# Performance work log

Hardware: AMD Instinct MI355X
Metric: run time of the kernel (lower is better)

Reference implementation:

```python
import jax, jax.numpy as jnp
import numpy as np

B, N, C, H = 128, 256, 512, 2
HD = C // H  # head_dim == num_patches == N by construction of the module's einsums
ALPHA = 3.0


def _safe_pow(x, p):
    # x >= 0 (post-relu); avoid 0**p corner issues while matching x**p exactly for x>0
    pos = x > 0
    return jnp.where(pos, jnp.where(pos, x, 1.0) ** p, 0.0)


def setup_inputs() -> dict:
    key = jax.random.key(0)
    ks = jax.random.split(key, 12)
    s = 0.02
    return {
        "x": jax.random.normal(ks[0], (B, N, C), jnp.float32),
        "Wq": jax.random.normal(ks[1], (C, C), jnp.float32) * s,
        "bq": jnp.zeros((C,), jnp.float32),
        "Wk": jax.random.normal(ks[2], (C, C), jnp.float32) * s,
        "bk": jnp.zeros((C,), jnp.float32),
        "Wvs": jax.random.normal(ks[3], (C, C // 2), jnp.float32) * s,
        "bvs": jnp.zeros((C // 2,), jnp.float32),
        "Wvc": jax.random.normal(ks[4], (C, C // 2), jnp.float32) * s,
        "bvc": jnp.zeros((C // 2,), jnp.float32),
        "power": jnp.ones((1, H, 1, HD), jnp.float32),
        "W_s": jax.random.uniform(ks[5], (N, HD // 2), jnp.float32),
        "W_c": jax.random.uniform(ks[6], (N, HD // 2), jnp.float32),
        "Wp": jax.random.normal(ks[7], (C, C), jnp.float32) * s,
        "bp": jnp.zeros((C,), jnp.float32),
    }


def reference(x, Wq, bq, Wk, bk, Wvs, bvs, Wvc, bvc, power, W_s, W_c, Wp, bp):
    b, n, c = x.shape
    h, hd = H, c // H
    # projections -> [B, H, N, hd] (or hd//2 for values)
    q = (x @ Wq + bq).reshape(b, n, h, hd).transpose(0, 2, 1, 3)
    k = (x @ Wk + bk).reshape(b, n, h, hd).transpose(0, 2, 1, 3)
    v_s = (x @ Wvs + bvs).reshape(b, n, h, hd // 2).transpose(0, 2, 1, 3)
    v_c = (x @ Wvc + bvc).reshape(b, n, h, hd // 2).transpose(0, 2, 1, 3)

    power_val = 1.0 + ALPHA * jax.nn.sigmoid(power)  # [1,H,1,hd]
    q_pos = _safe_pow(jax.nn.relu(q), power_val)
    q_neg = _safe_pow(jax.nn.relu(-q), power_val)
    k_pos = _safe_pow(jax.nn.relu(k), power_val)
    k_neg = _safe_pow(jax.nn.relu(-k), power_val)

    # kv_s = einsum(k_pos,v_s)+einsum(k_neg,v_s) == einsum(k_pos+k_neg, v_s); same for kv_c
    k_abs = k_pos + k_neg
    q_abs = q_pos + q_neg
    kv_s = jnp.einsum('bhnj,bhjd->bhnd', k_abs, v_s)
    q_s_context = jnp.einsum('bhni,bhid->bhnd', q_abs, kv_s)
    kv_c = jnp.einsum('bhnj,bhjd->bhnd', k_abs, v_c)
    q_c_context = jnp.einsum('bhni,bhid->bhnd', q_abs, kv_c)

    kp_sum = k_pos.sum(-1)  # [B,H,N]
    kn_sum = k_neg.sum(-1)
    denom_s = jnp.einsum('bhni,bhi->bhn', q_pos, kp_sum) + jnp.einsum('bhni,bhi->bhn', q_neg, kn_sum)
    denom_c = jnp.einsum('bhni,bhi->bhn', q_pos, kn_sum) + jnp.einsum('bhni,bhi->bhn', q_neg, kp_sum)

    attn_s = q_s_context / (denom_s[..., None] + 1e-6) * W_s  # W_s: [N, hd//2]
    attn_c = q_c_context / (denom_c[..., None] + 1e-6) * W_c

    out = jnp.concatenate([attn_s, attn_c], axis=-1)  # [B,H,N,hd]
    out = out.transpose(0, 2, 1, 3).reshape(b, n, c)
    return out @ Wp + bp
```

## Files before the change

### kernel.cpp

```cpp
#include <hip/hip_runtime.h>
#include <hip/hip_bf16.h>
#include <math.h>

typedef unsigned int u32;
typedef short bf16x8 __attribute__((ext_vector_type(8)));
typedef float f32x4 __attribute__((ext_vector_type(4)));
typedef u32 u32x4 __attribute__((ext_vector_type(4)));

__device__ __forceinline__ float bf2f(short s) {
    u32 u = ((u32)(unsigned short)s) << 16;
    return __builtin_bit_cast(float, u);
}
__device__ __forceinline__ short f2bf(float f) {
    u32 u = __builtin_bit_cast(u32, f);
    u32 r = u + 0x7fffu + ((u >> 16) & 1u);
    return (short)(r >> 16);
}
__device__ __forceinline__ float fast_log2(float x) {
    float r; asm volatile("v_log_f32 %0, %1" : "=v"(r) : "v"(x)); return r;
}
__device__ __forceinline__ float fast_exp2(float x) {
    float r; asm volatile("v_exp_f32 %0, %1" : "=v"(r) : "v"(x)); return r;
}
__device__ __forceinline__ void gload_lds16(const short* g, short* lds) {
    __builtin_amdgcn_global_load_lds(
        (const __attribute__((address_space(1))) u32*)g,
        (__attribute__((address_space(3))) u32*)lds, 16, 0, 0);
}
__device__ __forceinline__ bf16x8 stripsign(bf16x8 v) {
    u32x4 u = __builtin_bit_cast(u32x4, v);
    u &= 0x7fff7fffu;
    return __builtin_bit_cast(bf16x8, u);
}

struct P {
    const float* bcat; const float* pcol;
    short* qa; short* ka;
    short* vt; short* kvt;
    const float* dsb; const float* dcb; const float* Ws; const float* Wc;
    short* Y; float* out;
};

__global__ void k_pack(const float* __restrict__ Wq, const float* __restrict__ Wk,
                       const float* __restrict__ Wvs, const float* __restrict__ Wvc,
                       const float* __restrict__ Wp,
                       const float* __restrict__ bq, const float* __restrict__ bk,
                       const float* __restrict__ bvs, const float* __restrict__ bvc,
                       const float* __restrict__ bp, const float* __restrict__ power,
                       short* __restrict__ WcatT, float* __restrict__ bcat, float* __restrict__ pcol)
{
    int i = blockIdx.x * 256 + threadIdx.x;
    int r = i >> 9, k = i & 511;
    float w;
    if (r < 512)       w = Wq[k * 512 + r];
    else if (r < 1024) w = Wk[k * 512 + (r - 512)];
    else if (r < 1536) {
        int rr = r - 1024; int h = rr >> 8; int d = rr & 255;
        w = (d < 128) ? Wvs[k * 256 + h * 128 + d] : Wvc[k * 256 + h * 128 + (d - 128)];
    } else             w = Wp[k * 512 + (r - 1536)];
    WcatT[i] = f2bf(w);

    if (i < 2048) {
        float bb;
        if (i < 512)       bb = bq[i];
        else if (i < 1024) bb = bk[i - 512];
        else if (i < 1536) {
            int rr = i - 1024; int h = rr >> 8; int d = rr & 255;
            bb = (d < 128) ? bvs[h * 128 + d] : bvc[h * 128 + (d - 128)];
        } else             bb = bp[i - 1536];
        bcat[i] = bb;
    }
    if (i < 512) pcol[i] = 1.0f + 3.0f / (1.0f + expf(-power[i]));
}

__global__ void k_cast(const float* __restrict__ x, short* __restrict__ xb)
{
    int i = blockIdx.x * 256 + threadIdx.x;
    float4 v = ((const float4*)x)[i];
    short4 s;
    s.x = f2bf(v.x); s.y = f2bf(v.y); s.z = f2bf(v.z); s.w = f2bf(v.w);
    ((short4*)xb)[i] = s;
}

__global__ void k_ksum(const short* __restrict__ ka,
                       float* __restrict__ kpsum, float* __restrict__ knsum)
{
    int gid = blockIdx.x * 256 + threadIdx.x;
    int gw = gid >> 6;
    int lane = gid & 63;
    short4 a4 = ((const short4*)(ka + ((size_t)gw << 8)))[lane];
    short aa[4] = {a4.x, a4.y, a4.z, a4.w};
    float sp = 0.f, sn = 0.f;
#pragma unroll
    for (int j = 0; j < 4; ++j) {
        float a = fabsf(bf2f(aa[j]));
        if (((unsigned short)aa[j] >> 15) == 0) sp += a; else sn += a;
    }
#pragma unroll
    for (int m = 1; m < 64; m <<= 1) { sp += __shfl_xor(sp, m, 64); sn += __shfl_xor(sn, m, 64); }
    if (lane == 0) { kpsum[gw] = sp; knsum[gw] = sn; }
}

__global__ void k_denom(const short* __restrict__ qa,
                        const float* __restrict__ kpsum, const float* __restrict__ knsum,
                        float* __restrict__ dsb, float* __restrict__ dcb)
{
    int gid = blockIdx.x * 256 + threadIdx.x;
    int gw = gid >> 6;
    int lane = gid & 63;
    int bhl = gw >> 8;
    short4 q4 = ((const short4*)(qa + ((size_t)gw << 8)))[lane];
    float4 kp4 = ((const float4*)(kpsum + ((size_t)bhl << 8)))[lane];
    float4 kn4 = ((const float4*)(knsum + ((size_t)bhl << 8)))[lane];
    short qq[4] = {q4.x, q4.y, q4.z, q4.w};
    float kp[4] = {kp4.x, kp4.y, kp4.z, kp4.w};
    float kn[4] = {kn4.x, kn4.y, kn4.z, kn4.w};
    float ss = 0.f, sc = 0.f;
#pragma unroll
    for (int j = 0; j < 4; ++j) {
        float a = fabsf(bf2f(qq[j]));
        if (((unsigned short)qq[j] >> 15) == 0) { ss += a * kp[j]; sc += a * kn[j]; }
        else                                    { ss += a * kn[j]; sc += a * kp[j]; }
    }
#pragma unroll
    for (int m = 1; m < 64; m <<= 1) { ss += __shfl_xor(ss, m, 64); sc += __shfl_xor(sc, m, 64); }
    if (lane == 0) { dsb[gw] = ss; dcb[gw] = sc; }
}

#define MODE_QK  0
#define MODE_VT  1
#define MODE_KV  2
#define MODE_CTX 3
#define MODE_OUT 4

template <int MODE>
__launch_bounds__(256, 4)
__global__ void gemm_nt(const short* __restrict__ Ag, const short* __restrict__ Bg,
                        int M, int N, int K, int tilesN, P p)
{
    __shared__ short As[128 * 64];
    __shared__ short Bs[128 * 64];

    const int nwg = gridDim.x * gridDim.y;
    const int s = blockIdx.y * gridDim.x + blockIdx.x;
    const int cpx = nwg >> 3;
    const int lin = (s & 7) * cpx + (s >> 3);

    int tm, tn, bhl;
    if (MODE == MODE_KV || MODE == MODE_CTX) {
        bhl = lin >> 2;
        int rem = lin & 3;
        tm = rem / tilesN; tn = rem % tilesN;
    } else {
        bhl = 0;
        tm = lin / tilesN; tn = lin % tilesN;
    }

    const short* A = Ag;
    const short* B = Bg;
    if (MODE == MODE_KV || MODE == MODE_CTX) {
        A += (size_t)bhl << 16;
        B += (size_t)bhl << 16;
    }
    constexpr bool stripA = (MODE == MODE_CTX);
    constexpr bool stripB = (MODE == MODE_KV);

    const int t = threadIdx.x;
    const int lane = t & 63;
    const int w = t >> 6;
    const int wr = w >> 1, wc = w & 1;

    f32x4 acc[4][4];
#pragma unroll
    for (int i = 0; i < 4; ++i)
#pragma unroll
        for (int j = 0; j < 4; ++j) acc[i][j] = 0.f;

    const int nkt = K >> 6;
    for (int kt = 0; kt < nkt; ++kt) {
#pragma unroll
        for (int q4i = 0; q4i < 4; ++q4i) {
            int seg = w * 4 + q4i;
            int r = seg * 8 + (lane >> 3);
            int c = (lane & 7) ^ (r & 7);
            const short* srcA = A + (size_t)(tm * 128 + r) * K + kt * 64 + c * 8;
            const short* srcB = B + (size_t)(tn * 128 + r) * K + kt * 64 + c * 8;
            gload_lds16(srcA, &As[seg * 512]);
            gload_lds16(srcB, &Bs[seg * 512]);
        }
        __syncthreads();
#pragma unroll
        for (int kk = 0; kk < 2; ++kk) {
            bf16x8 af[4], bfr[4];
#pragma unroll
            for (int mt = 0; mt < 4; ++mt) {
                int row = wr * 64 + mt * 16 + (lane & 15);
                int ch = kk * 4 + (lane >> 4);
                af[mt] = *(const bf16x8*)(&As[row * 64 + ((ch ^ (row & 7)) << 3)]);
                if constexpr (stripA) af[mt] = stripsign(af[mt]);
            }
#pragma unroll
            for (int nt = 0; nt < 4; ++nt) {
                int row = wc * 64 + nt * 16 + (lane & 15);
                int ch = kk * 4 + (lane >> 4);
                bfr[nt] = *(const bf16x8*)(&Bs[row * 64 + ((ch ^ (row & 7)) << 3)]);
                if constexpr (stripB) bfr[nt] = stripsign(bfr[nt]);
            }
#pragma unroll
            for (int mt = 0; mt < 4; ++mt)
#pragma unroll
                for (int nt = 0; nt < 4; ++nt)
                    acc[mt][nt] = __builtin_amdgcn_mfma_f32_16x16x32_bf16(af[mt], bfr[nt], acc[mt][nt], 0, 0, 0);
        }
        __syncthreads();
    }

#pragma unroll
    for (int mt = 0; mt < 4; ++mt) {
#pragma unroll
        for (int nt = 0; nt < 4; ++nt) {
#pragma unroll
            for (int r = 0; r < 4; ++r) {
                int row = tm * 128 + wr * 64 + mt * 16 + (lane >> 4) * 4 + r;
                int col = tn * 128 + wc * 64 + nt * 16 + (lane & 15);
                float v = acc[mt][nt][r];
                if (MODE == MODE_QK) {
                    v += p.bcat[col];
                    float pw = p.pcol[col & 511];
                    float a = (v != 0.0f) ? fast_exp2(pw * fast_log2(fabsf(v))) : 0.0f;
                    unsigned short sa = (unsigned short)f2bf(a);
                    sa |= (unsigned short)((__builtin_bit_cast(u32, v) >> 16) & 0x8000u);
                    int bl = row >> 8, n = row & 255;
                    int h = (col >> 8) & 1;
                    size_t idx = ((size_t)((bl * 2 + h) * 256 + n) << 8) + (col & 255);
                    if (col < 512) p.qa[idx] = (short)sa;
                    else           p.ka[idx] = (short)sa;
                } else if (MODE == MODE_VT) {
                    v += p.bcat[1024 + row];
                    int h = row >> 8, d = row & 255;
                    int bl = col >> 8, n = col & 255;
                    p.vt[((size_t)((bl * 2 + h) * 256 + d) << 8) + n] = f2bf(v);
                } else if (MODE == MODE_KV) {
                    p.kvt[((size_t)bhl << 16) + (row << 8) + col] = f2bf(v);
                } else if (MODE == MODE_CTX) {
                    int n = row, d = col;
                    float den = ((d < 128) ? p.dsb : p.dcb)[bhl * 256 + n] + 1e-6f;
                    float wgt = (d < 128) ? p.Ws[n * 128 + d] : p.Wc[n * 128 + (d - 128)];
                    v = v / den * wgt;
                    int bl = bhl >> 1, h = bhl & 1;
                    p.Y[((size_t)(bl * 256 + n) << 9) + h * 256 + d] = f2bf(v);
                } else {
                    v += p.bcat[1536 + col];
                    p.out[((size_t)row << 9) + col] = v;
                }
            }
        }
    }
}

extern "C" void kernel_launch(void* const* d_in, const int* in_sizes, int n_in,
                              void* d_out, int out_size, void* d_ws, size_t ws_size,
                              hipStream_t stream)
{
    const float* x     = (const float*)d_in[0];
    const float* Wq    = (const float*)d_in[1];
    const float* bq    = (const float*)d_in[2];
    const float* Wk    = (const float*)d_in[3];
    const float* bk    = (const float*)d_in[4];
    const float* Wvs   = (const float*)d_in[5];
    const float* bvs   = (const float*)d_in[6];
    const float* Wvc   = (const float*)d_in[7];
    const float* bvc   = (const float*)d_in[8];
    const float* power = (const float*)d_in[9];
    const float* Ws    = (const float*)d_in[10];
    const float* Wc    = (const float*)d_in[11];
    const float* Wp    = (const float*)d_in[12];
    const float* bp    = (const float*)d_in[13];
    (void)in_sizes; (void)n_in; (void)out_size; (void)ws_size;

    char* ws = (char*)d_ws;
    size_t off = 0;
    auto alloc = [&](size_t bytes) { void* pp = ws + off; off += (bytes + 255) & ~(size_t)255; return pp; };
    short* Wcat = (short*)alloc(2097152);
    float* bcat = (float*)alloc(8192);
    float* pcol = (float*)alloc(2048);
    short* xb   = (short*)alloc(33554432);
    short* qa   = (short*)alloc(33554432);
    short* ka   = (short*)alloc(33554432);
    short* vt   = (short*)alloc(33554432);
    short* kvt  = (short*)alloc(33554432);
    float* kpsum= (float*)alloc(262144);
    float* knsum= (float*)alloc(262144);
    float* dsb  = (float*)alloc(262144);
    float* dcb  = (float*)alloc(262144);

    P p{};
    p.bcat = bcat; p.pcol = pcol;
    p.qa = qa; p.ka = ka;
    p.vt = vt; p.kvt = kvt;
    p.dsb = dsb; p.dcb = dcb; p.Ws = Ws; p.Wc = Wc;
    p.Y = xb; p.out = nullptr;

    k_pack<<<4096, 256, 0, stream>>>(Wq, Wk, Wvs, Wvc, Wp, bq, bk, bvs, bvc, bp, power, Wcat, bcat, pcol);

    k_cast<<<16384, 256, 0, stream>>>(x, xb);

    gemm_nt<MODE_QK><<<dim3(2048, 1), 256, 0, stream>>>(xb, Wcat, 32768, 1024, 512, 8, p);

    gemm_nt<MODE_VT><<<dim3(1024, 1), 256, 0, stream>>>(Wcat + 1024 * 512, xb, 512, 32768, 512, 256, p);

    gemm_nt<MODE_KV><<<dim3(4, 256), 256, 0, stream>>>(vt, ka, 256, 256, 256, 2, p);

    k_ksum<<<16384, 256, 0, stream>>>(ka, kpsum, knsum);

    k_denom<<<16384, 256, 0, stream>>>(qa, kpsum, knsum, dsb, dcb);

    gemm_nt<MODE_CTX><<<dim3(4, 256), 256, 0, stream>>>(qa, kvt, 256, 256, 256, 2, p);

    P po = p;
    po.out = (float*)d_out;
    gemm_nt<MODE_OUT><<<dim3(1024, 1), 256, 0, stream>>>(xb, Wcat + 1536 * 512, 32768, 512, 512, 4, po);
}
```

Measured before the change: 219.5 us.

## Add double-buffered 256x256 GEMM kernel for the projection GEMMs

Adds a new gemm_big kernel that uses 512 threads, 256x256 output tiles and double-buffered LDS staging, so global-to-LDS loads for the next K tiles overlap with MFMA work. The large QK, VT and output projection GEMMs move to it, while the batched per-head KV/CTX GEMMs stay on the original kernel. The aim is more data reuse per tile and hidden load latency. In exchange, the grid has fewer workgroups, register and LDS use per workgroup is higher (64KB LDS), and the kernel hardcodes K=512.

```diff
diff --git a/kernel.cpp b/kernel.cpp
--- a/kernel.cpp
+++ b/kernel.cpp
@@ -134,96 +134,99 @@
 #define MODE_OUT 4
 
 template <int MODE>
-__launch_bounds__(256, 4)
-__global__ void gemm_nt(const short* __restrict__ Ag, const short* __restrict__ Bg,
-                        int M, int N, int K, int tilesN, P p)
-{
-    __shared__ short As[128 * 64];
-    __shared__ short Bs[128 * 64];
-
-    const int nwg = gridDim.x * gridDim.y;
-    const int s = blockIdx.y * gridDim.x + blockIdx.x;
+__launch_bounds__(512, 2)
+__global__ void gemm_big(const short* __restrict__ Ag, const short* __restrict__ Bg,
+                         int tilesN, P p)
+{
+    __shared__ short As[2][256 * 64];
+    __shared__ short Bs[2][256 * 64];
+
+    const int nwg = gridDim.x;
+    const int s = blockIdx.x;
     const int cpx = nwg >> 3;
     const int lin = (s & 7) * cpx + (s >> 3);
-
-    int tm, tn, bhl;
-    if (MODE == MODE_KV || MODE == MODE_CTX) {
-        bhl = lin >> 2;
-        int rem = lin & 3;
-        tm = rem / tilesN; tn = rem % tilesN;
-    } else {
-        bhl = 0;
-        tm = lin / tilesN; tn = lin % tilesN;
-    }
-
-    const short* A = Ag;
-    const short* B = Bg;
-    if (MODE == MODE_KV || MODE == MODE_CTX) {
-        A += (size_t)bhl << 16;
-        B += (size_t)bhl << 16;
-    }
-    constexpr bool stripA = (MODE == MODE_CTX);
-    constexpr bool stripB = (MODE == MODE_KV);
+    const int tm = lin / tilesN, tn = lin % tilesN;
 
     const int t = threadIdx.x;
     const int lane = t & 63;
     const int w = t >> 6;
-    const int wr = w >> 1, wc = w & 1;
-
-    f32x4 acc[4][4];
-#pragma unroll
-    for (int i = 0; i < 4; ++i)
+    const int wr = w >> 2;
+    const int wc = w & 3;
+
+    const short* A = Ag + (size_t)tm * 256 * 512;
+    const short* B = Bg + (size_t)tn * 256 * 512;
+
+    auto stage = [&](const short* G, short* lds, int kt) {
+#pragma unroll
+        for (int i = 0; i < 4; ++i) {
+            int rl = i * 64 + w * 8 + (lane >> 3);
+            int c = (lane & 7) ^ (rl & 7);
+            gload_lds16(G + (size_t)rl * 512 + kt * 64 + c * 8,
+                        lds + (i * 64 + w * 8) * 64);
+        }
+    };
+
+    f32x4 acc[8][4];
+#pragma unroll
+    for (int i = 0; i < 8; ++i)
 #pragma unroll
         for (int j = 0; j < 4; ++j) acc[i][j] = 0.f;
 
-    const int nkt = K >> 6;
-    for (int kt = 0; kt < nkt; ++kt) {
-#pragma unroll
-        for (int q4i = 0; q4i < 4; ++q4i) {
-            int seg = w * 4 + q4i;
-            int r = seg * 8 + (lane >> 3);
-            int c = (lane & 7) ^ (r & 7);
-            const short* srcA = A + (size_t)(tm * 128 + r) * K + kt * 64 + c * 8;
-            const short* srcB = B + (size_t)(tn * 128 + r) * K + kt * 64 + c * 8;
-            gload_lds16(srcA, &As[seg * 512]);
-            gload_lds16(srcB, &Bs[seg * 512]);
-        }
-        __syncthreads();
+    stage(A, &As[0][0], 0); stage(B, &Bs[0][0], 0);
+    stage(A, &As[1][0], 1); stage(B, &Bs[1][0], 1);
+    asm volatile("s_waitcnt vmcnt(8)" ::: "memory");
+    __builtin_amdgcn_sched_barrier(0);
+    __builtin_amdgcn_s_barrier();
+
+    for (int kt = 0; kt < 8; ++kt) {
+        const int cur = kt & 1;
+        bf16x8 a[2][8], b[2][4];
 #pragma unroll
         for (int kk = 0; kk < 2; ++kk) {
-            bf16x8 af[4], bfr[4];
-#pragma unroll
-            for (int mt = 0; mt < 4; ++mt) {
-                int row = wr * 64 + mt * 16 + (lane & 15);
+#pragma unroll
+            for (int mf = 0; mf < 8; ++mf) {
+                int row = wr * 128 + mf * 16 + (lane & 15);
                 int ch = kk * 4 + (lane >> 4);
-                af[mt] = *(const bf16x8*)(&As[row * 64 + ((ch ^ (row & 7)) << 3)]);
-                if constexpr (stripA) af[mt] = stripsign(af[mt]);
-            }
-#pragma unroll
-            for (int nt = 0; nt < 4; ++nt) {
-                int row = wc * 64 + nt * 16 + (lane & 15);
+                a[kk][mf] = *(const bf16x8*)&As[cur][row * 64 + ((ch ^ (row & 7)) << 3)];
+            }
+#pragma unroll
+            for (int nf = 0; nf < 4; ++nf) {
+                int row = wc * 64 + nf * 16 + (lane & 15);
                 int ch = kk * 4 + (lane >> 4);
-                bfr[nt] = *(const bf16x8*)(&Bs[row * 64 + ((ch ^ (row & 7)) << 3)]);
-                if constexpr (stripB) bfr[nt] = stripsign(bfr[nt]);
-            }
-#pragma unroll
-            for (int mt = 0; mt < 4; ++mt)
-#pragma unroll
-                for (int nt = 0; nt < 4; ++nt)
-                    acc[mt][nt] = __builtin_amdgcn_mfma_f32_16x16x32_bf16(af[mt], bfr[nt], acc[mt][nt], 0, 0, 0);
-        }
-        __syncthreads();
-    }
-
-#pragma unroll
-    for (int mt = 0; mt < 4; ++mt) {
-#pragma unroll
-        for (int nt = 0; nt < 4; ++nt) {
+                b[kk][nf] = *(const bf16x8*)&Bs[cur][row * 64 + ((ch ^ (row & 7)) << 3)];
+            }
+        }
+        asm volatile("s_waitcnt lgkmcnt(0)" ::: "memory");
+        __builtin_amdgcn_sched_barrier(0);
+        __builtin_amdgcn_s_barrier();
+        __builtin_amdgcn_sched_barrier(0);
+        if (kt + 2 < 8) {
+            stage(A, &As[cur][0], kt + 2);
+            stage(B, &Bs[cur][0], kt + 2);
+        }
+        __builtin_amdgcn_sched_barrier(0);
+#pragma unroll
+        for (int kk = 0; kk < 2; ++kk)
+#pragma unroll
+            for (int mf = 0; mf < 8; ++mf)
+#pragma unroll
+                for (int nf = 0; nf < 4; ++nf)
+                    acc[mf][nf] = __builtin_amdgcn_mfma_f32_16x16x32_bf16(a[kk][mf], b[kk][nf], acc[mf][nf], 0, 0, 0);
+        if (kt + 2 < 8) { asm volatile("s_waitcnt vmcnt(8)" ::: "memory"); }
+        else            { asm volatile("s_waitcnt vmcnt(0)" ::: "memory"); }
+        __builtin_amdgcn_sched_barrier(0);
+        __builtin_amdgcn_s_barrier();
+    }
+
+#pragma unroll
+    for (int mf = 0; mf < 8; ++mf) {
+#pragma unroll
+        for (int nf = 0; nf < 4; ++nf) {
 #pragma unroll
             for (int r = 0; r < 4; ++r) {
-                int row = tm * 128 + wr * 64 + mt * 16 + (lane >> 4) * 4 + r;
-                int col = tn * 128 + wc * 64 + nt * 16 + (lane & 15);
-                float v = acc[mt][nt][r];
+                int row = tm * 256 + wr * 128 + mf * 16 + (lane >> 4) * 4 + r;
+                int col = tn * 256 + wc * 64 + nf * 16 + (lane & 15);
+                float v = acc[mf][nf][r];
                 if (MODE == MODE_QK) {
                     v += p.bcat[col];
                     float pw = p.pcol[col & 511];
@@ -240,18 +243,103 @@
                     int h = row >> 8, d = row & 255;
                     int bl = col >> 8, n = col & 255;
                     p.vt[((size_t)((bl * 2 + h) * 256 + d) << 8) + n] = f2bf(v);
-                } else if (MODE == MODE_KV) {
+                } else {
+                    v += p.bcat[1536 + col];
+                    p.out[((size_t)row << 9) + col] = v;
+                }
+            }
+        }
+    }
+}
+
+template <int MODE>
+__launch_bounds__(256, 4)
+__global__ void gemm_nt(const short* __restrict__ Ag, const short* __restrict__ Bg,
+                        int K, int tilesN, P p)
+{
+    __shared__ short As[128 * 64];
+    __shared__ short Bs[128 * 64];
+
+    const int nwg = gridDim.x * gridDim.y;
+    const int s = blockIdx.y * gridDim.x + blockIdx.x;
+    const int cpx = nwg >> 3;
+    const int lin = (s & 7) * cpx + (s >> 3);
+
+    const int bhl = lin >> 2;
+    const int rem = lin & 3;
+    const int tm = rem / tilesN, tn = rem % tilesN;
+
+    const short* A = Ag + ((size_t)bhl << 16);
+    const short* B = Bg + ((size_t)bhl << 16);
+    constexpr bool stripA = (MODE == MODE_CTX);
+    constexpr bool stripB = (MODE == MODE_KV);
+
+    const int t = threadIdx.x;
+    const int lane = t & 63;
+    const int w = t >> 6;
+    const int wr = w >> 1, wc = w & 1;
+
+    f32x4 acc[4][4];
+#pragma unroll
+    for (int i = 0; i < 4; ++i)
+#pragma unroll
+        for (int j = 0; j < 4; ++j) acc[i][j] = 0.f;
+
+    const int nkt = K >> 6;
+    for (int kt = 0; kt < nkt; ++kt) {
+#pragma unroll
+        for (int q4i = 0; q4i < 4; ++q4i) {
+            int seg = w * 4 + q4i;
+            int r = seg * 8 + (lane >> 3);
+            int c = (lane & 7) ^ (r & 7);
+            gload_lds16(A + (size_t)(tm * 128 + r) * K + kt * 64 + c * 8, &As[seg * 512]);
+            gload_lds16(B + (size_t)(tn * 128 + r) * K + kt * 64 + c * 8, &Bs[seg * 512]);
+        }
+        __syncthreads();
+#pragma unroll
+        for (int kk = 0; kk < 2; ++kk) {
+            bf16x8 af[4], bfr[4];
+#pragma unroll
+            for (int mt = 0; mt < 4; ++mt) {
+                int row = wr * 64 + mt * 16 + (lane & 15);
+                int ch = kk * 4 + (lane >> 4);
+                af[mt] = *(const bf16x8*)(&As[row * 64 + ((ch ^ (row & 7)) << 3)]);
+                if constexpr (stripA) af[mt] = stripsign(af[mt]);
+            }
+#pragma unroll
+            for (int nt = 0; nt < 4; ++nt) {
+                int row = wc * 64 + nt * 16 + (lane & 15);
+                int ch = kk * 4 + (lane >> 4);
+                bfr[nt] = *(const bf16x8*)(&Bs[row * 64 + ((ch ^ (row & 7)) << 3)]);
+                if constexpr (stripB) bfr[nt] = stripsign(bfr[nt]);
+            }
+#pragma unroll
+            for (int mt = 0; mt < 4; ++mt)
+#pragma unroll
+                for (int nt = 0; nt < 4; ++nt)
+                    acc[mt][nt] = __builtin_amdgcn_mfma_f32_16x16x32_bf16(af[mt], bfr[nt], acc[mt][nt], 0, 0, 0);
+        }
+        __syncthreads();
+    }
+
+#pragma unroll
+    for (int mt = 0; mt < 4; ++mt) {
+#pragma unroll
+        for (int nt = 0; nt < 4; ++nt) {
+#pragma unroll
+            for (int r = 0; r < 4; ++r) {
+                int row = tm * 128 + wr * 64 + mt * 16 + (lane >> 4) * 4 + r;
+                int col = tn * 128 + wc * 64 + nt * 16 + (lane & 15);
+                float v = acc[mt][nt][r];
+                if (MODE == MODE_KV) {
                     p.kvt[((size_t)bhl << 16) + (row << 8) + col] = f2bf(v);
-                } else if (MODE == MODE_CTX) {
+                } else {
                     int n = row, d = col;
                     float den = ((d < 128) ? p.dsb : p.dcb)[bhl * 256 + n] + 1e-6f;
                     float wgt = (d < 128) ? p.Ws[n * 128 + d] : p.Wc[n * 128 + (d - 128)];
                     v = v / den * wgt;
                     int bl = bhl >> 1, h = bhl & 1;
                     p.Y[((size_t)(bl * 256 + n) << 9) + h * 256 + d] = f2bf(v);
-                } else {
-                    v += p.bcat[1536 + col];
-                    p.out[((size_t)row << 9) + col] = v;
                 }
             }
         }
@@ -305,19 +393,18 @@
 
     k_cast<<<16384, 256, 0, stream>>>(x, xb);
 
-    gemm_nt<MODE_QK><<<dim3(2048, 1), 256, 0, stream>>>(xb, Wcat, 32768, 1024, 512, 8, p);
-
-    gemm_nt<MODE_VT><<<dim3(1024, 1), 256, 0, stream>>>(Wcat + 1024 * 512, xb, 512, 32768, 512, 256, p);
-
-    gemm_nt<MODE_KV><<<dim3(4, 256), 256, 0, stream>>>(vt, ka, 256, 256, 256, 2, p);
+    gemm_big<MODE_QK><<<512, 512, 0, stream>>>(xb, Wcat, 4, p);
+
+    gemm_big<MODE_VT><<<256, 512, 0, stream>>>(Wcat + 1024 * 512, xb, 128, p);
+
+    gemm_nt<MODE_KV><<<dim3(4, 256), 256, 0, stream>>>(vt, ka, 256, 2, p);
 
     k_ksum<<<16384, 256, 0, stream>>>(ka, kpsum, knsum);
-
     k_denom<<<16384, 256, 0, stream>>>(qa, kpsum, knsum, dsb, dcb);
 
-    gemm_nt<MODE_CTX><<<dim3(4, 256), 256, 0, stream>>>(qa, kvt, 256, 256, 256, 2, p);
+    gemm_nt<MODE_CTX><<<dim3(4, 256), 256, 0, stream>>>(qa, kvt, 256, 2, p);
 
     P po = p;
     po.out = (float*)d_out;
-    gemm_nt<MODE_OUT><<<dim3(1024, 1), 256, 0, stream>>>(xb, Wcat + 1536 * 512, 32768, 512, 512, 4, po);
-}
+    gemm_big<MODE_OUT><<<256, 512, 0, stream>>>(xb, Wcat + 1536 * 512, 2, po);
+}
```

New measurement: 291.6 us. 1.33x slower.

## Permute packed weight rows so GEMM epilogues emit vectorized stores

Applied to the files above, without the earlier changes.

The packed Q/K and output-projection weight rows are permuted inside each 64-row block. Each lane's four MFMA column tiles then map to four contiguous output columns, so the QK and OUT epilogues write short4 or float4 instead of scalar elements. The V-transpose GEMM swaps its operands so that consecutive tokens land in registers and can be stored as short4. Launch bounds go from 4 to 5 waves per SIMD, which may increase register pressure or spilling in exchange for occupancy.

```diff
diff --git a/kernel.cpp b/kernel.cpp
--- a/kernel.cpp
+++ b/kernel.cpp
@@ -51,13 +51,16 @@
 {
     int i = blockIdx.x * 256 + threadIdx.x;
     int r = i >> 9, k = i & 511;
+    int rs = r;
+    if (r < 1024 || r >= 1536)
+        rs = (r & ~63) | ((r & 15) << 2) | ((r >> 4) & 3);
     float w;
-    if (r < 512)       w = Wq[k * 512 + r];
-    else if (r < 1024) w = Wk[k * 512 + (r - 512)];
-    else if (r < 1536) {
-        int rr = r - 1024; int h = rr >> 8; int d = rr & 255;
+    if (rs < 512)       w = Wq[k * 512 + rs];
+    else if (rs < 1024) w = Wk[k * 512 + (rs - 512)];
+    else if (rs < 1536) {
+        int rr = rs - 1024; int h = rr >> 8; int d = rr & 255;
         w = (d < 128) ? Wvs[k * 256 + h * 128 + d] : Wvc[k * 256 + h * 128 + (d - 128)];
-    } else             w = Wp[k * 512 + (r - 1536)];
+    } else             w = Wp[k * 512 + (rs - 1536)];
     WcatT[i] = f2bf(w);
 
     if (i < 2048) {
@@ -134,9 +137,9 @@
 #define MODE_OUT 4
 
 template <int MODE>
-__launch_bounds__(256, 4)
+__launch_bounds__(256, 5)
 __global__ void gemm_nt(const short* __restrict__ Ag, const short* __restrict__ Bg,
-                        int M, int N, int K, int tilesN, P p)
+                        int K, int tilesN, P p)
 {
     __shared__ short As[128 * 64];
     __shared__ short Bs[128 * 64];
@@ -183,10 +186,8 @@
             int seg = w * 4 + q4i;
             int r = seg * 8 + (lane >> 3);
             int c = (lane & 7) ^ (r & 7);
-            const short* srcA = A + (size_t)(tm * 128 + r) * K + kt * 64 + c * 8;
-            const short* srcB = B + (size_t)(tn * 128 + r) * K + kt * 64 + c * 8;
-            gload_lds16(srcA, &As[seg * 512]);
-            gload_lds16(srcB, &Bs[seg * 512]);
+            gload_lds16(A + (size_t)(tm * 128 + r) * K + kt * 64 + c * 8, &As[seg * 512]);
+            gload_lds16(B + (size_t)(tn * 128 + r) * K + kt * 64 + c * 8, &Bs[seg * 512]);
         }
         __syncthreads();
 #pragma unroll
@@ -215,43 +216,81 @@
         __syncthreads();
     }
 
-#pragma unroll
-    for (int mt = 0; mt < 4; ++mt) {
-#pragma unroll
-        for (int nt = 0; nt < 4; ++nt) {
+    if (MODE == MODE_QK) {
+#pragma unroll
+        for (int mt = 0; mt < 4; ++mt) {
 #pragma unroll
             for (int r = 0; r < 4; ++r) {
-                int row = tm * 128 + wr * 64 + mt * 16 + (lane >> 4) * 4 + r;
-                int col = tn * 128 + wc * 64 + nt * 16 + (lane & 15);
-                float v = acc[mt][nt][r];
-                if (MODE == MODE_QK) {
-                    v += p.bcat[col];
-                    float pw = p.pcol[col & 511];
+                int n_g = tm * 128 + wr * 64 + mt * 16 + (lane >> 4) * 4 + r;
+                int l0  = tn * 128 + wc * 64 + (lane & 15) * 4;
+                short4 sv;
+#pragma unroll
+                for (int nt = 0; nt < 4; ++nt) {
+                    int lg = l0 + nt;
+                    float v = acc[mt][nt][r] + p.bcat[lg];
+                    float pw = p.pcol[lg & 511];
                     float a = (v != 0.0f) ? fast_exp2(pw * fast_log2(fabsf(v))) : 0.0f;
                     unsigned short sa = (unsigned short)f2bf(a);
                     sa |= (unsigned short)((__builtin_bit_cast(u32, v) >> 16) & 0x8000u);
-                    int bl = row >> 8, n = row & 255;
-                    int h = (col >> 8) & 1;
-                    size_t idx = ((size_t)((bl * 2 + h) * 256 + n) << 8) + (col & 255);
-                    if (col < 512) p.qa[idx] = (short)sa;
-                    else           p.ka[idx] = (short)sa;
-                } else if (MODE == MODE_VT) {
-                    v += p.bcat[1024 + row];
-                    int h = row >> 8, d = row & 255;
-                    int bl = col >> 8, n = col & 255;
-                    p.vt[((size_t)((bl * 2 + h) * 256 + d) << 8) + n] = f2bf(v);
-                } else if (MODE == MODE_KV) {
-                    p.kvt[((size_t)bhl << 16) + (row << 8) + col] = f2bf(v);
-                } else if (MODE == MODE_CTX) {
-                    int n = row, d = col;
-                    float den = ((d < 128) ? p.dsb : p.dcb)[bhl * 256 + n] + 1e-6f;
-                    float wgt = (d < 128) ? p.Ws[n * 128 + d] : p.Wc[n * 128 + (d - 128)];
-                    v = v / den * wgt;
-                    int bl = bhl >> 1, h = bhl & 1;
-                    p.Y[((size_t)(bl * 256 + n) << 9) + h * 256 + d] = f2bf(v);
-                } else {
-                    v += p.bcat[1536 + col];
-                    p.out[((size_t)row << 9) + col] = v;
+                    ((short*)&sv)[nt] = (short)sa;
+                }
+                int bl = n_g >> 8, n = n_g & 255;
+                int h = (l0 >> 8) & 1;
+                short* dst = (l0 < 512) ? p.qa : p.ka;
+                *(short4*)(dst + (((size_t)((bl * 2 + h) * 256 + n)) << 8) + (l0 & 255)) = sv;
+            }
+        }
+    } else if (MODE == MODE_VT) {
+#pragma unroll
+        for (int mt = 0; mt < 4; ++mt) {
+#pragma unroll
+            for (int nt = 0; nt < 4; ++nt) {
+                int d_g = tn * 128 + wc * 64 + nt * 16 + (lane & 15);
+                int n0  = tm * 128 + wr * 64 + mt * 16 + (lane >> 4) * 4;
+                float bias = p.bcat[1024 + d_g];
+                short4 sv;
+#pragma unroll
+                for (int r = 0; r < 4; ++r)
+                    ((short*)&sv)[r] = f2bf(acc[mt][nt][r] + bias);
+                int bl = n0 >> 8;
+                int h = d_g >> 8, d = d_g & 255;
+                *(short4*)(p.vt + (((size_t)((bl * 2 + h) * 256 + d)) << 8) + (n0 & 255)) = sv;
+            }
+        }
+    } else if (MODE == MODE_OUT) {
+#pragma unroll
+        for (int mt = 0; mt < 4; ++mt) {
+#pragma unroll
+            for (int r = 0; r < 4; ++r) {
+                int row_g = tm * 128 + wr * 64 + mt * 16 + (lane >> 4) * 4 + r;
+                int l0 = tn * 128 + wc * 64 + (lane & 15) * 4;
+                float4 fv;
+#pragma unroll
+                for (int nt = 0; nt < 4; ++nt)
+                    ((float*)&fv)[nt] = acc[mt][nt][r] + p.bcat[1536 + l0 + nt];
+                *(float4*)(p.out + ((size_t)row_g << 9) + l0) = fv;
+            }
+        }
+    } else {
+#pragma unroll
+        for (int mt = 0; mt < 4; ++mt) {
+#pragma unroll
+            for (int nt = 0; nt < 4; ++nt) {
+#pragma unroll
+                for (int r = 0; r < 4; ++r) {
+                    int row = tm * 128 + wr * 64 + mt * 16 + (lane >> 4) * 4 + r;
+                    int col = tn * 128 + wc * 64 + nt * 16 + (lane & 15);
+                    float v = acc[mt][nt][r];
+                    if (MODE == MODE_KV) {
+                        p.kvt[((size_t)bhl << 16) + (row << 8) + col] = f2bf(v);
+                    } else {
+                        int n = row, d = col;
+                        float den = ((d < 128) ? p.dsb : p.dcb)[bhl * 256 + n] + 1e-6f;
+                        float wgt = (d < 128) ? p.Ws[n * 128 + d] : p.Wc[n * 128 + (d - 128)];
+                        v = v / den * wgt;
+                        int bl = bhl >> 1, h = bhl & 1;
+                        p.Y[((size_t)(bl * 256 + n) << 9) + h * 256 + d] = f2bf(v);
+                    }
                 }
             }
         }
@@ -305,19 +344,18 @@
 
     k_cast<<<16384, 256, 0, stream>>>(x, xb);
 
-    gemm_nt<MODE_QK><<<dim3(2048, 1), 256, 0, stream>>>(xb, Wcat, 32768, 1024, 512, 8, p);
-
-    gemm_nt<MODE_VT><<<dim3(1024, 1), 256, 0, stream>>>(Wcat + 1024 * 512, xb, 512, 32768, 512, 256, p);
-
-    gemm_nt<MODE_KV><<<dim3(4, 256), 256, 0, stream>>>(vt, ka, 256, 256, 256, 2, p);
+    gemm_nt<MODE_QK><<<dim3(2048, 1), 256, 0, stream>>>(xb, Wcat, 512, 8, p);
+
+    gemm_nt<MODE_VT><<<dim3(1024, 1), 256, 0, stream>>>(xb, Wcat + 1024 * 512, 512, 4, p);
+
+    gemm_nt<MODE_KV><<<dim3(4, 256), 256, 0, stream>>>(vt, ka, 256, 2, p);
 
     k_ksum<<<16384, 256, 0, stream>>>(ka, kpsum, knsum);
-
     k_denom<<<16384, 256, 0, stream>>>(qa, kpsum, knsum, dsb, dcb);
 
-    gemm_nt<MODE_CTX><<<dim3(4, 256), 256, 0, stream>>>(qa, kvt, 256, 256, 256, 2, p);
+    gemm_nt<MODE_CTX><<<dim3(4, 256), 256, 0, stream>>>(qa, kvt, 256, 2, p);
 
     P po = p;
     po.out = (float*)d_out;
-    gemm_nt<MODE_OUT><<<dim3(1024, 1), 256, 0, stream>>>(xb, Wcat + 1536 * 512, 32768, 512, 512, 4, po);
-}
+    gemm_nt<MODE_OUT><<<dim3(1024, 1), 256, 0, stream>>>(xb, Wcat + 1536 * 512, 512, 4, po);
+}
```

New measurement: 454.8 us. 2.07x slower.
